# Performance work log

Hardware: AMD Instinct MI355X
Metric: run time of the kernel (lower is better)

Reference implementation:

```python
import jax, jax.numpy as jnp
import numpy as np

N_NODES = 100000
HIDDEN = 128


def _gcn_conv(x, edge_index, W, b, n_nodes):
    # PyG GCNConv with default symmetric normalization and self-loops.
    src, dst = edge_index[0], edge_index[1]
    loop = jnp.arange(n_nodes, dtype=src.dtype)
    src = jnp.concatenate([src, loop])
    dst = jnp.concatenate([dst, loop])
    # degree over destination nodes (edge weight = 1), self-loops included
    deg = jax.ops.segment_sum(jnp.ones_like(dst, dtype=x.dtype), dst,
                              num_segments=n_nodes)
    dinv = jax.lax.rsqrt(deg)  # deg >= 1 because of self-loops
    norm = dinv[src] * dinv[dst]  # [E+N]
    h = x @ W  # [N, 4H] linear transform first (d_in -> 4H)
    msg = norm[:, None] * h[src]  # [E+N, 4H]
    out = jax.ops.segment_sum(msg, dst, num_segments=n_nodes)
    return out + b


def setup_inputs() -> dict:
    key = jax.random.key(0)
    k1, k2, k3, k4, k5, k6 = jax.random.split(key, 6)
    n, h = N_NODES, HIDDEN
    x = jax.random.normal(k1, (n, h), dtype=jnp.float32)
    h_cur = jax.random.normal(k2, (n, h), dtype=jnp.float32)
    c_cur = jax.random.normal(k3, (n, h), dtype=jnp.float32)
    edge_index = jax.random.randint(k4, (2, 3200000), 0, n, dtype=jnp.int64)
    W = jax.random.normal(k5, (h, 4 * h), dtype=jnp.float32) / np.sqrt(h)
    b = jax.random.normal(k6, (4 * h,), dtype=jnp.float32) * 0.01
    return {"x": x, "edge_index": edge_index, "h_cur": h_cur,
            "c_cur": c_cur, "W": W, "b": b}


def reference(x, edge_index, h_cur, c_cur, W, b):
    combined = x + h_cur  # fused input + hidden add
    conv = _gcn_conv(combined, edge_index, W, b, x.shape[0])  # [N, 4H]
    cc_f = conv[:, :HIDDEN]  # first gate chunk (module returns cc_f only)
    return cc_f
```

## Files before the change

kernel.cpp:

```cpp
#include <hip/hip_runtime.h>
#include <hip/hip_bf16.h>

#define HID 128
#define BSH 6
#define MAXBUCK 2048
#define NSB 512
#define CAP 2816

__device__ __forceinline__ float b2f(unsigned short u) {
    union { unsigned i; float f; } v; v.i = ((unsigned)u) << 16; return v.f;
}
__device__ __forceinline__ unsigned short f2b(float f) {
    unsigned u = __float_as_uint(f);
    return (unsigned short)((u + 0x7fffu + ((u >> 16) & 1u)) >> 16);
}

__global__ __launch_bounds__(256) void histblk_kernel(const int* __restrict__ ei,
                                                      unsigned* __restrict__ hist,
                                                      int E, int n, int nbuck) {
    __shared__ unsigned h[MAXBUCK];
    for (int i = threadIdx.x; i < nbuck; i += 256) h[i] = 0u;
    __syncthreads();
    int blk = blockIdx.x;
    int chunk = (E + NSB - 1) / NSB;
    int beg = blk * chunk, end = min(E, beg + chunk);
    for (int i = beg + threadIdx.x; i < end; i += 256) {
        int dst = ei[(size_t)E + i];
        if ((unsigned)dst < (unsigned)n) atomicAdd(&h[dst >> BSH], 1u);
    }
    __syncthreads();
    for (int b = threadIdx.x; b < nbuck; b += 256)
        hist[(size_t)blk * nbuck + b] = h[b];
}

__global__ __launch_bounds__(256) void scan2d_kernel(const unsigned* __restrict__ hist,
                                                     unsigned* __restrict__ base_rel,
                                                     unsigned* __restrict__ bcount,
                                                     int nbuck) {
    int b = blockIdx.x;
    int t = threadIdx.x;
    unsigned v0 = hist[(size_t)(2 * t) * nbuck + b];
    unsigned v1 = hist[(size_t)(2 * t + 1) * nbuck + b];
    unsigned pair = v0 + v1;
    int lane = t & 63, w = t >> 6;
    unsigned x = pair;
    for (int d = 1; d < 64; d <<= 1) {
        unsigned y = __shfl_up(x, d, 64);
        if (lane >= d) x += y;
    }
    __shared__ unsigned wsum[4];
    if (lane == 63) wsum[w] = x;
    __syncthreads();
    unsigned add = 0;
    for (int ww = 0; ww < 4; ++ww) if (ww < w) add += wsum[ww];
    unsigned incl = x + add;
    unsigned excl = incl - pair;
    base_rel[(size_t)(2 * t) * nbuck + b] = excl;
    base_rel[(size_t)(2 * t + 1) * nbuck + b] = excl + v0;
    if (t == 255) bcount[b] = incl;
}

__global__ __launch_bounds__(1024) void bscan_kernel(const unsigned* __restrict__ bcount,
                                                     unsigned* __restrict__ boff,
                                                     int nbuck) {
    __shared__ unsigned sums[1024];
    int t = threadIdx.x;
    int chunk = (nbuck + 1023) >> 10;
    int beg = min(t * chunk, nbuck), end = min(beg + chunk, nbuck);
    unsigned local = 0;
    for (int i = beg; i < end; ++i) local += bcount[i];
    sums[t] = local;
    __syncthreads();
    for (int d = 1; d < 1024; d <<= 1) {
        unsigned v = (t >= d) ? sums[t - d] : 0u;
        __syncthreads();
        sums[t] += v;
        __syncthreads();
    }
    unsigned run = (t > 0) ? sums[t - 1] : 0u;
    for (int i = beg; i < end; ++i) { boff[i] = run; run += bcount[i]; }
    if (t == 1023) boff[nbuck] = sums[1023];
}

__global__ __launch_bounds__(256) void phase3_kernel(const int* __restrict__ ei,
                                                     const unsigned* __restrict__ boff,
                                                     const unsigned* __restrict__ base_rel,
                                                     unsigned* __restrict__ binned,
                                                     const float* __restrict__ x,
                                                     const float* __restrict__ hc,
                                                     const float* __restrict__ W,
                                                     unsigned short* __restrict__ hp,
                                                     int E, int n, int nbuck) {
    __shared__ union {
        unsigned cursor[MAXBUCK];
        float A[32 * 132];
    } sm;

    if (blockIdx.x < NSB) {
        int blk = blockIdx.x;
        for (int b = threadIdx.x; b < nbuck; b += 256)
            sm.cursor[b] = boff[b] + base_rel[(size_t)blk * nbuck + b];
        __syncthreads();
        int chunk = (E + NSB - 1) / NSB;
        int beg = blk * chunk, end = min(E, beg + chunk);
        for (int i = beg + threadIdx.x; i < end; i += 256) {
            int s = ei[i];
            int dst = ei[(size_t)E + i];
            if ((unsigned)dst >= (unsigned)n) continue;
            unsigned ss = (unsigned)min(max(s, 0), n - 1);
            unsigned slot = atomicAdd(&sm.cursor[dst >> BSH], 1u);
            binned[slot] = ss | ((unsigned)(dst & ((1 << BSH) - 1)) << 20);
        }
    } else {
        int tid = threadIdx.x;
        int r0 = (blockIdx.x - NSB) * 32;

        for (int i = tid; i < 1024; i += 256) {
            int row = i >> 5;
            int c4 = (i & 31) * 4;
            int grow = r0 + row;
            float4 v;
            if (grow < n) {
                float4 a = *(const float4*)(x + (size_t)grow * HID + c4);
                float4 bb = *(const float4*)(hc + (size_t)grow * HID + c4);
                v = make_float4(a.x + bb.x, a.y + bb.y, a.z + bb.z, a.w + bb.w);
            } else {
                v = make_float4(0.f, 0.f, 0.f, 0.f);
            }
            *(float4*)(&sm.A[row * 132 + c4]) = v;
        }
        __syncthreads();

        int cg = tid & 31;
        int c4 = cg * 4;
        int rg = tid >> 5;
        float acc[4][4];
#pragma unroll
        for (int r = 0; r < 4; ++r) {
            acc[r][0] = 0.f; acc[r][1] = 0.f; acc[r][2] = 0.f; acc[r][3] = 0.f;
        }

#pragma unroll 4
        for (int k = 0; k < 128; ++k) {
            float4 w = *(const float4*)(W + (size_t)k * 512 + c4);
#pragma unroll
            for (int r = 0; r < 4; ++r) {
                float a = sm.A[(rg * 4 + r) * 132 + k];
                acc[r][0] += a * w.x;
                acc[r][1] += a * w.y;
                acc[r][2] += a * w.z;
                acc[r][3] += a * w.w;
            }
        }

#pragma unroll
        for (int r = 0; r < 4; ++r) {
            int grow = r0 + rg * 4 + r;
            if (grow < n) {
                unsigned long long pack =
                    (unsigned long long)f2b(acc[r][0]) |
                    ((unsigned long long)f2b(acc[r][1]) << 16) |
                    ((unsigned long long)f2b(acc[r][2]) << 32) |
                    ((unsigned long long)f2b(acc[r][3]) << 48);
                *(unsigned long long*)(hp + (size_t)grow * HID + c4) = pack;
            }
        }
    }
}

__global__ __launch_bounds__(256) void csrlite_kernel(const unsigned* __restrict__ binned,
                                                      const unsigned* __restrict__ boff,
                                                      unsigned* __restrict__ off,
                                                      float* __restrict__ dinv, int n) {
    __shared__ unsigned hist[64];
    int b = blockIdx.x;
    int t = threadIdx.x;
    if (t < 64) hist[t] = 0u;
    __syncthreads();
    unsigned s0 = boff[b], s1 = boff[b + 1];
    for (unsigned j = s0 + t; j < s1; j += 256) atomicAdd(&hist[binned[j] >> 20], 1u);
    __syncthreads();
    if (t < 64) {
        unsigned cnt = hist[t];
        unsigned x = cnt;
        for (int d = 1; d < 64; d <<= 1) {
            unsigned v = __shfl_up(x, d, 64);
            if (t >= d) x += v;
        }
        unsigned excl = x - cnt;
        int node = (b << BSH) + t;
        if (node < n) {
            off[node] = s0 + excl;
            dinv[node] = rsqrtf((float)(cnt + 1u));
        }
    }
}

__global__ __launch_bounds__(256) void agg_merged_kernel(const unsigned* __restrict__ binned,
                                                         const unsigned* __restrict__ boff,
                                                         const unsigned* __restrict__ off,
                                                         const float* __restrict__ dinv,
                                                         const unsigned short* __restrict__ hp,
                                                         const float* __restrict__ bias,
                                                         float* __restrict__ out, int n) {
    __shared__ unsigned srcs_lds[CAP];
    __shared__ unsigned nodeoff[65];
    __shared__ unsigned cursor[64];
    __shared__ float sdinv[64];
    int b = blockIdx.x;
    int tid = threadIdx.x;
    unsigned s0 = boff[b], s1 = boff[b + 1];
    unsigned cnt = s1 - s0;
    int node0 = b << BSH;

    if (tid < 64) {
        int node = node0 + tid;
        unsigned o = (node < n) ? off[node] : s1;
        nodeoff[tid] = o - s0;
        cursor[tid] = o - s0;
        sdinv[tid] = (node < n) ? dinv[node] : 0.f;
    }
    if (tid == 64) nodeoff[64] = cnt;
    __syncthreads();

    if (cnt <= CAP) {
        for (unsigned j = s0 + tid; j < s1; j += 256) {
            unsigned p = binned[j];
            unsigned slot = atomicAdd(&cursor[p >> 20], 1u);
            srcs_lds[slot] = p & 0xFFFFFu;
        }
        __syncthreads();

        int w = tid >> 6, lane = tid & 63;
        int c = lane * 2;
        for (int nl = w * 16; nl < w * 16 + 16; ++nl) {
            int node = node0 + nl;
            if (node >= n) break;
            unsigned beg = nodeoff[nl], end2 = nodeoff[nl + 1];
            float ax = 0.f, ay = 0.f;
            unsigned i = beg;
            for (; i + 8 <= end2; i += 8) {
                unsigned s[8]; float wd[8]; ushort2 v[8];
#pragma unroll
                for (int j = 0; j < 8; ++j) s[j] = srcs_lds[i + j];
#pragma unroll
                for (int j = 0; j < 8; ++j) wd[j] = dinv[s[j]];
#pragma unroll
                for (int j = 0; j < 8; ++j) v[j] = *(const ushort2*)(hp + ((size_t)s[j] << 7) + c);
#pragma unroll
                for (int j = 0; j < 8; ++j) { ax += wd[j] * b2f(v[j].x); ay += wd[j] * b2f(v[j].y); }
            }
            if (i < end2) {
                unsigned last = end2 - 1;
                unsigned s[8]; float wd[8]; ushort2 v[8];
#pragma unroll
                for (int j = 0; j < 8; ++j) {
                    unsigned jj = i + j;
                    s[j] = srcs_lds[jj < end2 ? jj : last];
                    wd[j] = (jj < end2) ? 1.f : 0.f;
                }
#pragma unroll
                for (int j = 0; j < 8; ++j) wd[j] *= dinv[s[j]];
#pragma unroll
                for (int j = 0; j < 8; ++j) v[j] = *(const ushort2*)(hp + ((size_t)s[j] << 7) + c);
#pragma unroll
                for (int j = 0; j < 8; ++j) { ax += wd[j] * b2f(v[j].x); ay += wd[j] * b2f(v[j].y); }
            }
            float dd = sdinv[nl];
            ushort2 hd = *(const ushort2*)(hp + ((size_t)node << 7) + c);
            ax += dd * b2f(hd.x);
            ay += dd * b2f(hd.y);
            float2 bb = *(const float2*)(bias + c);
            float2 res = make_float2(dd * ax + bb.x, dd * ay + bb.y);
            *(float2*)(out + ((size_t)node << 7) + c) = res;
        }
    } else {
        for (int idx = tid; idx < 64 * HID; idx += 256) {
            int ndl = idx >> 7, col = idx & (HID - 1);
            int node = node0 + ndl;
            if (node < n) {
                float dd = sdinv[ndl];
                out[((size_t)node << 7) + col] = dd * dd * b2f(hp[((size_t)node << 7) + col]) + bias[col];
            }
        }
        __syncthreads();
        if (tid < 64) {
            int c = tid * 2;
            for (unsigned j = s0; j < s1; ++j) {
                unsigned p = binned[j];
                unsigned dl = p >> 20, s = p & 0xFFFFFu;
                float wsc = dinv[s] * sdinv[dl];
                ushort2 v = *(const ushort2*)(hp + ((size_t)s << 7) + c);
                float2* o = (float2*)(out + ((size_t)(node0 + dl) << 7) + c);
                float2 cur = *o;
                cur.x += wsc * b2f(v.x);
                cur.y += wsc * b2f(v.y);
                *o = cur;
            }
        }
    }
}

extern "C" void kernel_launch(void* const* d_in, const int* in_sizes, int n_in,
                              void* d_out, int out_size, void* d_ws, size_t ws_size,
                              hipStream_t stream) {
    const float* x = (const float*)d_in[0];
    const int* ei = (const int*)d_in[1];
    const float* hc = (const float*)d_in[2];
    const float* W = (const float*)d_in[4];
    const float* b = (const float*)d_in[5];
    float* out = (float*)d_out;

    int n = in_sizes[0] / HID;
    int E = in_sizes[1] / 2;
    int nbuck = (n + 63) >> BSH;

    char* ws = (char*)d_ws;
    unsigned* bcount = (unsigned*)(ws);
    unsigned* boff   = (unsigned*)(ws + 8192);
    unsigned* off    = (unsigned*)(ws + 24576);
    float*    dinv   = (float*)   (ws + 424576);
    unsigned* binned = (unsigned*)(ws + 824576);
    unsigned short* hp = (unsigned short*)(ws + 13624576);

    unsigned* hist     = (unsigned*)d_out;
    unsigned* base_rel = hist + (size_t)NSB * nbuck;

    histblk_kernel<<<NSB, 256, 0, stream>>>(ei, hist, E, n, nbuck);
    scan2d_kernel<<<nbuck, 256, 0, stream>>>(hist, base_rel, bcount, nbuck);
    bscan_kernel<<<1, 1024, 0, stream>>>(bcount, boff, nbuck);

    int gemm_blocks = (n + 31) / 32;
    phase3_kernel<<<NSB + gemm_blocks, 256, 0, stream>>>(ei, boff, base_rel, binned,
                                                         x, hc, W, hp, E, n, nbuck);
    csrlite_kernel<<<nbuck, 256, 0, stream>>>(binned, boff, off, dinv, n);
    agg_merged_kernel<<<nbuck, 256, 0, stream>>>(binned, boff, off, dinv, hp, b, out, n);
}
```

Baseline: 246.6 us.

## Sort edge chunks locally in LDS before coalesced scatter; enlarge GEMM row tile

Each binning block now counts, scans and sorts its edge chunk into shared memory by bucket, then writes out contiguous runs to global memory. This replaces scattered single-word global writes with mostly coalesced ones. The sort blocks drop from 512 to 256 so each chunk (12500 edges) fits the 12800-entry LDS buffer. The GEMM path also processes 64 rows per block with 8 rows per thread, which reuses each W load over more rows. The larger shared-memory footprint (~75KB) and extra passes over the edges may reduce occupancy, and the binary search per output element adds work.

```diff
diff --git a/kernel.cpp b/kernel.cpp
--- a/kernel.cpp
+++ b/kernel.cpp
@@ -4,7 +4,8 @@
 #define HID 128
 #define BSH 6
 #define MAXBUCK 2048
-#define NSB 512
+#define NSB 256
+#define SORTCAP 12800
 #define CAP 2816
 
 __device__ __forceinline__ float b2f(unsigned short u) {
@@ -39,11 +40,9 @@
                                                      int nbuck) {
     int b = blockIdx.x;
     int t = threadIdx.x;
-    unsigned v0 = hist[(size_t)(2 * t) * nbuck + b];
-    unsigned v1 = hist[(size_t)(2 * t + 1) * nbuck + b];
-    unsigned pair = v0 + v1;
+    unsigned v = hist[(size_t)t * nbuck + b];
     int lane = t & 63, w = t >> 6;
-    unsigned x = pair;
+    unsigned x = v;
     for (int d = 1; d < 64; d <<= 1) {
         unsigned y = __shfl_up(x, d, 64);
         if (lane >= d) x += y;
@@ -54,9 +53,7 @@
     unsigned add = 0;
     for (int ww = 0; ww < 4; ++ww) if (ww < w) add += wsum[ww];
     unsigned incl = x + add;
-    unsigned excl = incl - pair;
-    base_rel[(size_t)(2 * t) * nbuck + b] = excl;
-    base_rel[(size_t)(2 * t + 1) * nbuck + b] = excl + v0;
+    base_rel[(size_t)t * nbuck + b] = incl - v;
     if (t == 255) bcount[b] = incl;
 }
 
@@ -82,40 +79,100 @@
     if (t == 1023) boff[nbuck] = sums[1023];
 }
 
-__global__ __launch_bounds__(256) void phase3_kernel(const int* __restrict__ ei,
-                                                     const unsigned* __restrict__ boff,
-                                                     const unsigned* __restrict__ base_rel,
-                                                     unsigned* __restrict__ binned,
-                                                     const float* __restrict__ x,
-                                                     const float* __restrict__ hc,
-                                                     const float* __restrict__ W,
-                                                     unsigned short* __restrict__ hp,
-                                                     int E, int n, int nbuck) {
+__global__ __launch_bounds__(256) void binsort_kernel(const int* __restrict__ ei,
+                                                      const unsigned* __restrict__ boff,
+                                                      const unsigned* __restrict__ base_rel,
+                                                      unsigned* __restrict__ binned,
+                                                      const float* __restrict__ x,
+                                                      const float* __restrict__ hc,
+                                                      const float* __restrict__ W,
+                                                      unsigned short* __restrict__ hp,
+                                                      int E, int n, int nbuck) {
     __shared__ union {
-        unsigned cursor[MAXBUCK];
-        float A[32 * 132];
+        struct {
+            unsigned sorted[SORTCAP];
+            unsigned lexcl[MAXBUCK + 1];
+            unsigned cursor[MAXBUCK];
+            unsigned gbase[MAXBUCK];
+        } bs;
+        float A[64 * 132];
     } sm;
 
+    int tid = threadIdx.x;
     if (blockIdx.x < NSB) {
         int blk = blockIdx.x;
-        for (int b = threadIdx.x; b < nbuck; b += 256)
-            sm.cursor[b] = boff[b] + base_rel[(size_t)blk * nbuck + b];
-        __syncthreads();
         int chunk = (E + NSB - 1) / NSB;
         int beg = blk * chunk, end = min(E, beg + chunk);
-        for (int i = beg + threadIdx.x; i < end; i += 256) {
-            int s = ei[i];
-            int dst = ei[(size_t)E + i];
-            if ((unsigned)dst >= (unsigned)n) continue;
-            unsigned ss = (unsigned)min(max(s, 0), n - 1);
-            unsigned slot = atomicAdd(&sm.cursor[dst >> BSH], 1u);
-            binned[slot] = ss | ((unsigned)(dst & ((1 << BSH) - 1)) << 20);
+
+        if (end - beg <= SORTCAP) {
+            for (int b = tid; b < nbuck; b += 256) sm.bs.cursor[b] = 0u;
+            __syncthreads();
+            for (int i = beg + tid; i < end; i += 256) {
+                int dst = ei[(size_t)E + i];
+                if ((unsigned)dst < (unsigned)n) atomicAdd(&sm.bs.cursor[dst >> BSH], 1u);
+            }
+            __syncthreads();
+            int K = (nbuck + 255) / 256;
+            int b0 = tid * K, b1 = min(b0 + K, nbuck);
+            unsigned partial = 0;
+            for (int b = b0; b < b1; ++b) partial += sm.bs.cursor[b];
+            int lane = tid & 63, w = tid >> 6;
+            unsigned xs = partial;
+            for (int d = 1; d < 64; d <<= 1) {
+                unsigned y = __shfl_up(xs, d, 64);
+                if (lane >= d) xs += y;
+            }
+            __shared__ unsigned wsum[4];
+            if (lane == 63) wsum[w] = xs;
+            __syncthreads();
+            unsigned add = 0;
+            for (int ww = 0; ww < 4; ++ww) if (ww < w) add += wsum[ww];
+            unsigned run = xs + add - partial;
+            for (int b = b0; b < b1; ++b) {
+                unsigned cnt_b = sm.bs.cursor[b];
+                sm.bs.lexcl[b] = run;
+                sm.bs.gbase[b] = boff[b] + base_rel[(size_t)blk * nbuck + b];
+                sm.bs.cursor[b] = run;
+                run += cnt_b;
+            }
+            if (tid == 255) sm.bs.lexcl[nbuck] = xs + add;
+            __syncthreads();
+            for (int i = beg + tid; i < end; i += 256) {
+                int s = ei[i];
+                int dst = ei[(size_t)E + i];
+                if ((unsigned)dst >= (unsigned)n) continue;
+                unsigned ss = (unsigned)min(max(s, 0), n - 1);
+                unsigned slot = atomicAdd(&sm.bs.cursor[dst >> BSH], 1u);
+                sm.bs.sorted[slot] = ss | ((unsigned)(dst & ((1 << BSH) - 1)) << 20);
+            }
+            __syncthreads();
+            unsigned cnt = sm.bs.lexcl[nbuck];
+            for (unsigned i = tid; i < cnt; i += 256) {
+                int lo = 0, hi = nbuck - 1;
+                while (lo < hi) {
+                    int mid = (lo + hi + 1) >> 1;
+                    if (sm.bs.lexcl[mid] <= i) lo = mid; else hi = mid - 1;
+                }
+                unsigned gpos = sm.bs.gbase[lo] + (i - sm.bs.lexcl[lo]);
+                binned[gpos] = sm.bs.sorted[i];
+            }
+        } else {
+            for (int b = tid; b < nbuck; b += 256)
+                sm.bs.cursor[b] = boff[b] + base_rel[(size_t)blk * nbuck + b];
+            __syncthreads();
+            for (int i = beg + tid; i < end; i += 256) {
+                int s = ei[i];
+                int dst = ei[(size_t)E + i];
+                if ((unsigned)dst >= (unsigned)n) continue;
+                unsigned ss = (unsigned)min(max(s, 0), n - 1);
+                unsigned slot = atomicAdd(&sm.bs.cursor[dst >> BSH], 1u);
+                binned[slot] = ss | ((unsigned)(dst & ((1 << BSH) - 1)) << 20);
+            }
         }
     } else {
-        int tid = threadIdx.x;
-        int r0 = (blockIdx.x - NSB) * 32;
-
-        for (int i = tid; i < 1024; i += 256) {
+        int r0 = (blockIdx.x - NSB) * 64;
+
+        for (int i = tid; i < 2048; i += 256) {
             int row = i >> 5;
             int c4 = (i & 31) * 4;
             int grow = r0 + row;
@@ -134,9 +191,9 @@
         int cg = tid & 31;
         int c4 = cg * 4;
         int rg = tid >> 5;
-        float acc[4][4];
-#pragma unroll
-        for (int r = 0; r < 4; ++r) {
+        float acc[8][4];
+#pragma unroll
+        for (int r = 0; r < 8; ++r) {
             acc[r][0] = 0.f; acc[r][1] = 0.f; acc[r][2] = 0.f; acc[r][3] = 0.f;
         }
 
@@ -144,8 +201,8 @@
         for (int k = 0; k < 128; ++k) {
             float4 w = *(const float4*)(W + (size_t)k * 512 + c4);
 #pragma unroll
-            for (int r = 0; r < 4; ++r) {
-                float a = sm.A[(rg * 4 + r) * 132 + k];
+            for (int r = 0; r < 8; ++r) {
+                float a = sm.A[(rg * 8 + r) * 132 + k];
                 acc[r][0] += a * w.x;
                 acc[r][1] += a * w.y;
                 acc[r][2] += a * w.z;
@@ -154,8 +211,8 @@
         }
 
 #pragma unroll
-        for (int r = 0; r < 4; ++r) {
-            int grow = r0 + rg * 4 + r;
+        for (int r = 0; r < 8; ++r) {
+            int grow = r0 + rg * 8 + r;
             if (grow < n) {
                 unsigned long long pack =
                     (unsigned long long)f2b(acc[r][0]) |
@@ -330,9 +387,9 @@
     scan2d_kernel<<<nbuck, 256, 0, stream>>>(hist, base_rel, bcount, nbuck);
     bscan_kernel<<<1, 1024, 0, stream>>>(bcount, boff, nbuck);
 
-    int gemm_blocks = (n + 31) / 32;
-    phase3_kernel<<<NSB + gemm_blocks, 256, 0, stream>>>(ei, boff, base_rel, binned,
-                                                         x, hc, W, hp, E, n, nbuck);
+    int gemm_blocks = (n + 63) / 64;
+    binsort_kernel<<<NSB + gemm_blocks, 256, 0, stream>>>(ei, boff, base_rel, binned,
+                                                          x, hc, W, hp, E, n, nbuck);
     csrlite_kernel<<<nbuck, 256, 0, stream>>>(binned, boff, off, dinv, n);
     agg_merged_kernel<<<nbuck, 256, 0, stream>>>(binned, boff, off, dinv, hp, b, out, n);
 }
```

Measured after the change: 268.6 us. 1.09x slower.

## Regroup edges into 128-node buckets and fuse histogram with GEMM

Applied to the files above, without the earlier changes.

Buckets grow from 64 to 128 destination nodes, and the histogram pass now runs in the same launch as the GEMM blocks, while the scatter becomes its own kernel. The per-node CSR offset kernel is dropped: dinv is computed from local counts, and the aggregation kernel builds its per-node offsets in LDS with a two-wave scan. The GEMM tile doubles to 64 rows per block with 8 accumulator rows per thread, and the number of partition blocks halves. This moves the GEMM off the scatter's critical path and removes the global offset array, at the cost of a larger LDS footprint (CAPG 4608) and more register pressure in the GEMM.

```diff
diff --git a/kernel.cpp b/kernel.cpp
--- a/kernel.cpp
+++ b/kernel.cpp
@@ -2,10 +2,10 @@
 #include <hip/hip_bf16.h>
 
 #define HID 128
-#define BSH 6
-#define MAXBUCK 2048
-#define NSB 512
-#define CAP 2816
+#define NGR_SH 7
+#define MAXGRP 1024
+#define NSB 256
+#define CAPG 4608
 
 __device__ __forceinline__ float b2f(unsigned short u) {
     union { unsigned i; float f; } v; v.i = ((unsigned)u) << 16; return v.f;
@@ -15,107 +15,34 @@
     return (unsigned short)((u + 0x7fffu + ((u >> 16) & 1u)) >> 16);
 }
 
-__global__ __launch_bounds__(256) void histblk_kernel(const int* __restrict__ ei,
-                                                      unsigned* __restrict__ hist,
-                                                      int E, int n, int nbuck) {
-    __shared__ unsigned h[MAXBUCK];
-    for (int i = threadIdx.x; i < nbuck; i += 256) h[i] = 0u;
-    __syncthreads();
-    int blk = blockIdx.x;
-    int chunk = (E + NSB - 1) / NSB;
-    int beg = blk * chunk, end = min(E, beg + chunk);
-    for (int i = beg + threadIdx.x; i < end; i += 256) {
-        int dst = ei[(size_t)E + i];
-        if ((unsigned)dst < (unsigned)n) atomicAdd(&h[dst >> BSH], 1u);
-    }
-    __syncthreads();
-    for (int b = threadIdx.x; b < nbuck; b += 256)
-        hist[(size_t)blk * nbuck + b] = h[b];
-}
-
-__global__ __launch_bounds__(256) void scan2d_kernel(const unsigned* __restrict__ hist,
-                                                     unsigned* __restrict__ base_rel,
-                                                     unsigned* __restrict__ bcount,
-                                                     int nbuck) {
-    int b = blockIdx.x;
-    int t = threadIdx.x;
-    unsigned v0 = hist[(size_t)(2 * t) * nbuck + b];
-    unsigned v1 = hist[(size_t)(2 * t + 1) * nbuck + b];
-    unsigned pair = v0 + v1;
-    int lane = t & 63, w = t >> 6;
-    unsigned x = pair;
-    for (int d = 1; d < 64; d <<= 1) {
-        unsigned y = __shfl_up(x, d, 64);
-        if (lane >= d) x += y;
-    }
-    __shared__ unsigned wsum[4];
-    if (lane == 63) wsum[w] = x;
-    __syncthreads();
-    unsigned add = 0;
-    for (int ww = 0; ww < 4; ++ww) if (ww < w) add += wsum[ww];
-    unsigned incl = x + add;
-    unsigned excl = incl - pair;
-    base_rel[(size_t)(2 * t) * nbuck + b] = excl;
-    base_rel[(size_t)(2 * t + 1) * nbuck + b] = excl + v0;
-    if (t == 255) bcount[b] = incl;
-}
-
-__global__ __launch_bounds__(1024) void bscan_kernel(const unsigned* __restrict__ bcount,
-                                                     unsigned* __restrict__ boff,
-                                                     int nbuck) {
-    __shared__ unsigned sums[1024];
-    int t = threadIdx.x;
-    int chunk = (nbuck + 1023) >> 10;
-    int beg = min(t * chunk, nbuck), end = min(beg + chunk, nbuck);
-    unsigned local = 0;
-    for (int i = beg; i < end; ++i) local += bcount[i];
-    sums[t] = local;
-    __syncthreads();
-    for (int d = 1; d < 1024; d <<= 1) {
-        unsigned v = (t >= d) ? sums[t - d] : 0u;
-        __syncthreads();
-        sums[t] += v;
-        __syncthreads();
-    }
-    unsigned run = (t > 0) ? sums[t - 1] : 0u;
-    for (int i = beg; i < end; ++i) { boff[i] = run; run += bcount[i]; }
-    if (t == 1023) boff[nbuck] = sums[1023];
-}
-
-__global__ __launch_bounds__(256) void phase3_kernel(const int* __restrict__ ei,
-                                                     const unsigned* __restrict__ boff,
-                                                     const unsigned* __restrict__ base_rel,
-                                                     unsigned* __restrict__ binned,
-                                                     const float* __restrict__ x,
-                                                     const float* __restrict__ hc,
-                                                     const float* __restrict__ W,
-                                                     unsigned short* __restrict__ hp,
-                                                     int E, int n, int nbuck) {
+__global__ __launch_bounds__(256) void histgemm_kernel(const int* __restrict__ ei,
+                                                       unsigned* __restrict__ hist,
+                                                       const float* __restrict__ x,
+                                                       const float* __restrict__ hc,
+                                                       const float* __restrict__ W,
+                                                       unsigned short* __restrict__ hp,
+                                                       int E, int n, int ngroups) {
     __shared__ union {
-        unsigned cursor[MAXBUCK];
-        float A[32 * 132];
+        unsigned h[MAXGRP];
+        float A[64 * 132];
     } sm;
+    int tid = threadIdx.x;
 
     if (blockIdx.x < NSB) {
-        int blk = blockIdx.x;
-        for (int b = threadIdx.x; b < nbuck; b += 256)
-            sm.cursor[b] = boff[b] + base_rel[(size_t)blk * nbuck + b];
+        for (int g = tid; g < ngroups; g += 256) sm.h[g] = 0u;
         __syncthreads();
         int chunk = (E + NSB - 1) / NSB;
-        int beg = blk * chunk, end = min(E, beg + chunk);
-        for (int i = beg + threadIdx.x; i < end; i += 256) {
-            int s = ei[i];
+        int beg = blockIdx.x * chunk, end = min(E, beg + chunk);
+        for (int i = beg + tid; i < end; i += 256) {
             int dst = ei[(size_t)E + i];
-            if ((unsigned)dst >= (unsigned)n) continue;
-            unsigned ss = (unsigned)min(max(s, 0), n - 1);
-            unsigned slot = atomicAdd(&sm.cursor[dst >> BSH], 1u);
-            binned[slot] = ss | ((unsigned)(dst & ((1 << BSH) - 1)) << 20);
-        }
+            if ((unsigned)dst < (unsigned)n) atomicAdd(&sm.h[dst >> NGR_SH], 1u);
+        }
+        __syncthreads();
+        for (int g = tid; g < ngroups; g += 256)
+            hist[(size_t)blockIdx.x * ngroups + g] = sm.h[g];
     } else {
-        int tid = threadIdx.x;
-        int r0 = (blockIdx.x - NSB) * 32;
-
-        for (int i = tid; i < 1024; i += 256) {
+        int r0 = (blockIdx.x - NSB) * 64;
+        for (int i = tid; i < 2048; i += 256) {
             int row = i >> 5;
             int c4 = (i & 31) * 4;
             int grow = r0 + row;
@@ -134,28 +61,26 @@
         int cg = tid & 31;
         int c4 = cg * 4;
         int rg = tid >> 5;
-        float acc[4][4];
-#pragma unroll
-        for (int r = 0; r < 4; ++r) {
+        float acc[8][4];
+#pragma unroll
+        for (int r = 0; r < 8; ++r) {
             acc[r][0] = 0.f; acc[r][1] = 0.f; acc[r][2] = 0.f; acc[r][3] = 0.f;
         }
-
 #pragma unroll 4
         for (int k = 0; k < 128; ++k) {
             float4 w = *(const float4*)(W + (size_t)k * 512 + c4);
 #pragma unroll
-            for (int r = 0; r < 4; ++r) {
-                float a = sm.A[(rg * 4 + r) * 132 + k];
+            for (int r = 0; r < 8; ++r) {
+                float a = sm.A[(rg * 8 + r) * 132 + k];
                 acc[r][0] += a * w.x;
                 acc[r][1] += a * w.y;
                 acc[r][2] += a * w.z;
                 acc[r][3] += a * w.w;
             }
         }
-
-#pragma unroll
-        for (int r = 0; r < 4; ++r) {
-            int grow = r0 + rg * 4 + r;
+#pragma unroll
+        for (int r = 0; r < 8; ++r) {
+            int grow = r0 + rg * 8 + r;
             if (grow < n) {
                 unsigned long long pack =
                     (unsigned long long)f2b(acc[r][0]) |
@@ -168,72 +93,146 @@
     }
 }
 
-__global__ __launch_bounds__(256) void csrlite_kernel(const unsigned* __restrict__ binned,
-                                                      const unsigned* __restrict__ boff,
-                                                      unsigned* __restrict__ off,
-                                                      float* __restrict__ dinv, int n) {
-    __shared__ unsigned hist[64];
-    int b = blockIdx.x;
+__global__ __launch_bounds__(256) void scan2d_kernel(const unsigned* __restrict__ hist,
+                                                     unsigned* __restrict__ base_rel,
+                                                     unsigned* __restrict__ gcount,
+                                                     int ngroups) {
+    int g = blockIdx.x;
     int t = threadIdx.x;
-    if (t < 64) hist[t] = 0u;
-    __syncthreads();
-    unsigned s0 = boff[b], s1 = boff[b + 1];
-    for (unsigned j = s0 + t; j < s1; j += 256) atomicAdd(&hist[binned[j] >> 20], 1u);
-    __syncthreads();
-    if (t < 64) {
-        unsigned cnt = hist[t];
-        unsigned x = cnt;
-        for (int d = 1; d < 64; d <<= 1) {
-            unsigned v = __shfl_up(x, d, 64);
-            if (t >= d) x += v;
-        }
-        unsigned excl = x - cnt;
-        int node = (b << BSH) + t;
-        if (node < n) {
-            off[node] = s0 + excl;
-            dinv[node] = rsqrtf((float)(cnt + 1u));
-        }
-    }
-}
-
-__global__ __launch_bounds__(256) void agg_merged_kernel(const unsigned* __restrict__ binned,
-                                                         const unsigned* __restrict__ boff,
-                                                         const unsigned* __restrict__ off,
-                                                         const float* __restrict__ dinv,
-                                                         const unsigned short* __restrict__ hp,
-                                                         const float* __restrict__ bias,
-                                                         float* __restrict__ out, int n) {
-    __shared__ unsigned srcs_lds[CAP];
-    __shared__ unsigned nodeoff[65];
-    __shared__ unsigned cursor[64];
-    __shared__ float sdinv[64];
-    int b = blockIdx.x;
+    unsigned v = hist[(size_t)t * ngroups + g];
+    int lane = t & 63, w = t >> 6;
+    unsigned x = v;
+    for (int d = 1; d < 64; d <<= 1) {
+        unsigned y = __shfl_up(x, d, 64);
+        if (lane >= d) x += y;
+    }
+    __shared__ unsigned wsum[4];
+    if (lane == 63) wsum[w] = x;
+    __syncthreads();
+    unsigned add = 0;
+    for (int ww = 0; ww < 4; ++ww) if (ww < w) add += wsum[ww];
+    unsigned incl = x + add;
+    base_rel[(size_t)t * ngroups + g] = incl - v;
+    if (t == 255) gcount[g] = incl;
+}
+
+__global__ __launch_bounds__(1024) void gscan_kernel(const unsigned* __restrict__ gcount,
+                                                     unsigned* __restrict__ gboff,
+                                                     int ngroups) {
+    __shared__ unsigned sums[1024];
+    int t = threadIdx.x;
+    int chunk = (ngroups + 1023) >> 10;
+    int beg = min(t * chunk, ngroups), end = min(beg + chunk, ngroups);
+    unsigned local = 0;
+    for (int i = beg; i < end; ++i) local += gcount[i];
+    sums[t] = local;
+    __syncthreads();
+    for (int d = 1; d < 1024; d <<= 1) {
+        unsigned v = (t >= d) ? sums[t - d] : 0u;
+        __syncthreads();
+        sums[t] += v;
+        __syncthreads();
+    }
+    unsigned run = (t > 0) ? sums[t - 1] : 0u;
+    for (int i = beg; i < end; ++i) { gboff[i] = run; run += gcount[i]; }
+    if (t == 1023) gboff[ngroups] = sums[1023];
+}
+
+__global__ __launch_bounds__(256) void gscatter_kernel(const int* __restrict__ ei,
+                                                       const unsigned* __restrict__ gboff,
+                                                       const unsigned* __restrict__ base_rel,
+                                                       unsigned* __restrict__ grouped,
+                                                       int E, int n, int ngroups) {
+    __shared__ unsigned cursor[MAXGRP];
+    int blk = blockIdx.x;
     int tid = threadIdx.x;
-    unsigned s0 = boff[b], s1 = boff[b + 1];
+    for (int g = tid; g < ngroups; g += 256)
+        cursor[g] = gboff[g] + base_rel[(size_t)blk * ngroups + g];
+    __syncthreads();
+    int chunk = (E + NSB - 1) / NSB;
+    int beg = blk * chunk, end = min(E, beg + chunk);
+    for (int i = beg + tid; i < end; i += 256) {
+        int s = ei[i];
+        int dst = ei[(size_t)E + i];
+        if ((unsigned)dst >= (unsigned)n) continue;
+        unsigned ss = (unsigned)min(max(s, 0), n - 1);
+        unsigned slot = atomicAdd(&cursor[dst >> NGR_SH], 1u);
+        grouped[slot] = ss | ((unsigned)(dst & ((1 << NGR_SH) - 1)) << 17);
+    }
+}
+
+__global__ __launch_bounds__(256) void dinvg_kernel(const unsigned* __restrict__ grouped,
+                                                    const unsigned* __restrict__ gboff,
+                                                    float* __restrict__ dinv, int n) {
+    __shared__ unsigned lcnt[128];
+    int g = blockIdx.x;
+    int t = threadIdx.x;
+    if (t < 128) lcnt[t] = 0u;
+    __syncthreads();
+    unsigned s0 = gboff[g], s1 = gboff[g + 1];
+    for (unsigned j = s0 + t; j < s1; j += 256) atomicAdd(&lcnt[grouped[j] >> 17], 1u);
+    __syncthreads();
+    if (t < 128) {
+        int node = (g << NGR_SH) + t;
+        if (node < n) dinv[node] = rsqrtf((float)(lcnt[t] + 1u));
+    }
+}
+
+__global__ __launch_bounds__(256) void aggsort_kernel(const unsigned* __restrict__ grouped,
+                                                      const unsigned* __restrict__ gboff,
+                                                      const float* __restrict__ dinv,
+                                                      const unsigned short* __restrict__ hp,
+                                                      const float* __restrict__ bias,
+                                                      float* __restrict__ out, int n) {
+    __shared__ unsigned srcs_lds[CAPG];
+    __shared__ unsigned nodeoff[129];
+    __shared__ unsigned cursor[128];
+    __shared__ float sdinv[128];
+    __shared__ unsigned wtot[2];
+    int g = blockIdx.x;
+    int tid = threadIdx.x;
+    unsigned s0 = gboff[g], s1 = gboff[g + 1];
     unsigned cnt = s1 - s0;
-    int node0 = b << BSH;
-
-    if (tid < 64) {
+    int node0 = g << NGR_SH;
+
+    if (tid < 128) {
         int node = node0 + tid;
-        unsigned o = (node < n) ? off[node] : s1;
-        nodeoff[tid] = o - s0;
-        cursor[tid] = o - s0;
         sdinv[tid] = (node < n) ? dinv[node] : 0.f;
-    }
-    if (tid == 64) nodeoff[64] = cnt;
-    __syncthreads();
-
-    if (cnt <= CAP) {
+        cursor[tid] = 0u;
+    }
+    __syncthreads();
+
+    if (cnt <= CAPG) {
+        for (unsigned j = s0 + tid; j < s1; j += 256) atomicAdd(&cursor[grouped[j] >> 17], 1u);
+        __syncthreads();
+        if (tid < 128) {
+            unsigned v = cursor[tid];
+            int lane = tid & 63, w = tid >> 6;
+            unsigned x = v;
+            for (int d = 1; d < 64; d <<= 1) {
+                unsigned y = __shfl_up(x, d, 64);
+                if (lane >= d) x += y;
+            }
+            if (lane == 63) wtot[w] = x;
+            __syncthreads();
+            unsigned excl = x - v + ((w == 1) ? wtot[0] : 0u);
+            nodeoff[tid] = excl;
+            cursor[tid] = excl;
+            if (tid == 127) nodeoff[128] = cnt;
+        } else {
+            __syncthreads();
+        }
+        __syncthreads();
         for (unsigned j = s0 + tid; j < s1; j += 256) {
-            unsigned p = binned[j];
-            unsigned slot = atomicAdd(&cursor[p >> 20], 1u);
-            srcs_lds[slot] = p & 0xFFFFFu;
+            unsigned p = grouped[j];
+            unsigned slot = atomicAdd(&cursor[p >> 17], 1u);
+            srcs_lds[slot] = p & 0x1FFFFu;
         }
         __syncthreads();
 
         int w = tid >> 6, lane = tid & 63;
         int c = lane * 2;
-        for (int nl = w * 16; nl < w * 16 + 16; ++nl) {
+        for (int nl = w * 32; nl < w * 32 + 32; ++nl) {
             int node = node0 + nl;
             if (node >= n) break;
             unsigned beg = nodeoff[nl], end2 = nodeoff[nl + 1];
@@ -275,7 +274,7 @@
             *(float2*)(out + ((size_t)node << 7) + c) = res;
         }
     } else {
-        for (int idx = tid; idx < 64 * HID; idx += 256) {
+        for (int idx = tid; idx < 128 * HID; idx += 256) {
             int ndl = idx >> 7, col = idx & (HID - 1);
             int node = node0 + ndl;
             if (node < n) {
@@ -287,8 +286,8 @@
         if (tid < 64) {
             int c = tid * 2;
             for (unsigned j = s0; j < s1; ++j) {
-                unsigned p = binned[j];
-                unsigned dl = p >> 20, s = p & 0xFFFFFu;
+                unsigned p = grouped[j];
+                unsigned dl = p >> 17, s = p & 0x1FFFFu;
                 float wsc = dinv[s] * sdinv[dl];
                 ushort2 v = *(const ushort2*)(hp + ((size_t)s << 7) + c);
                 float2* o = (float2*)(out + ((size_t)(node0 + dl) << 7) + c);
@@ -313,26 +312,23 @@
 
     int n = in_sizes[0] / HID;
     int E = in_sizes[1] / 2;
-    int nbuck = (n + 63) >> BSH;
+    int ngroups = (n + 127) >> NGR_SH;
 
     char* ws = (char*)d_ws;
-    unsigned* bcount = (unsigned*)(ws);
-    unsigned* boff   = (unsigned*)(ws + 8192);
-    unsigned* off    = (unsigned*)(ws + 24576);
-    float*    dinv   = (float*)   (ws + 424576);
-    unsigned* binned = (unsigned*)(ws + 824576);
-    unsigned short* hp = (unsigned short*)(ws + 13624576);
+    unsigned* gcount = (unsigned*)(ws);
+    unsigned* gboff  = (unsigned*)(ws + 8192);
+    float*    dinv   = (float*)   (ws + 16384);
+    unsigned* grouped= (unsigned*)(ws + 416384);
+    unsigned short* hp = (unsigned short*)(ws + 13216384);
 
     unsigned* hist     = (unsigned*)d_out;
-    unsigned* base_rel = hist + (size_t)NSB * nbuck;
-
-    histblk_kernel<<<NSB, 256, 0, stream>>>(ei, hist, E, n, nbuck);
-    scan2d_kernel<<<nbuck, 256, 0, stream>>>(hist, base_rel, bcount, nbuck);
-    bscan_kernel<<<1, 1024, 0, stream>>>(bcount, boff, nbuck);
-
-    int gemm_blocks = (n + 31) / 32;
-    phase3_kernel<<<NSB + gemm_blocks, 256, 0, stream>>>(ei, boff, base_rel, binned,
-                                                         x, hc, W, hp, E, n, nbuck);
-    csrlite_kernel<<<nbuck, 256, 0, stream>>>(binned, boff, off, dinv, n);
-    agg_merged_kernel<<<nbuck, 256, 0, stream>>>(binned, boff, off, dinv, hp, b, out, n);
-}
+    unsigned* base_rel = hist + (size_t)NSB * ngroups;
+
+    int gemm_blocks = (n + 63) / 64;
+    histgemm_kernel<<<NSB + gemm_blocks, 256, 0, stream>>>(ei, hist, x, hc, W, hp, E, n, ngroups);
+    scan2d_kernel<<<ngroups, 256, 0, stream>>>(hist, base_rel, gcount, ngroups);
+    gscan_kernel<<<1, 1024, 0, stream>>>(gcount, gboff, ngroups);
+    gscatter_kernel<<<NSB, 256, 0, stream>>>(ei, gboff, base_rel, grouped, E, n, ngroups);
+    dinvg_kernel<<<ngroups, 256, 0, stream>>>(grouped, gboff, dinv, n);
+    aggsort_kernel<<<ngroups, 256, 0, stream>>>(grouped, gboff, dinv, hp, b, out, n);
+}
```

Result: no change. 247.3 us (+0.3%).
